# Performance work log

Measured on AMD Instinct MI355X. Metric: run time of the kernel, lower is better.

## Reference

```python
import jax, jax.numpy as jnp
import numpy as np

ATOM_DIMS = [119, 5, 12, 12, 10, 6, 6, 2, 2]  # OGB full_atom_feature_dims
N, E, D, H, L, C, G = 50000, 400000, 64, 4, 3, 10, 512
NEG_SLOPE = 0.2


def setup_inputs() -> dict:
    key = jax.random.key(0)
    ks = jax.random.split(key, 12)
    total_vocab = sum(ATOM_DIMS)  # 174
    inp = {
        "nodes_features": jax.random.randint(ks[0], (N, 9), 0, 2),
        "edges_connectivity": jax.random.randint(ks[1], (2, E), 0, N),
        "batch": jnp.sort(jax.random.randint(ks[2], (N,), 0, G)),
        "atom_emb": jax.random.normal(ks[3], (total_vocab, D), jnp.float32) * 0.1,
        # GATv2 per-layer params: lin_l (source), lin_r (target), attention vec, out bias
        "Wl": jax.random.normal(ks[4], (L, D, H * D), jnp.float32) * 0.05,
        "bl": jnp.zeros((L, H * D), jnp.float32),
        "Wr": jax.random.normal(ks[5], (L, D, H * D), jnp.float32) * 0.05,
        "br": jnp.zeros((L, H * D), jnp.float32),
        "att": jax.random.normal(ks[6], (L, H, D), jnp.float32) * 0.1,
        "gat_bias": jnp.zeros((L, D), jnp.float32),
        "Wc": jax.random.normal(ks[7], (D, C), jnp.float32) * 0.05,
        "bc": jnp.zeros((C,), jnp.float32),
    }
    return inp


def reference(nodes_features, edges_connectivity, batch, atom_emb,
              Wl, bl, Wr, br, att, gat_bias, Wc, bc):
    # --- AtomEncoder: sum of 9 categorical embeddings (tables concatenated) ---
    offsets = jnp.asarray(np.cumsum([0] + ATOM_DIMS[:-1]), dtype=nodes_features.dtype)
    x = atom_emb[nodes_features + offsets[None, :]].sum(axis=1)  # [N, D]

    # --- add self-loops (GATv2Conv default add_self_loops=True) ---
    loops = jnp.arange(N, dtype=edges_connectivity.dtype)
    src = jnp.concatenate([edges_connectivity[0], loops])  # [E+N]
    dst = jnp.concatenate([edges_connectivity[1], loops])

    for l in range(L):
        xl = (x @ Wl[l] + bl[l]).reshape(N, H, D)  # source transform
        xr = (x @ Wr[l] + br[l]).reshape(N, H, D)  # target transform
        m = jax.nn.leaky_relu(xl[src] + xr[dst], NEG_SLOPE)      # [E+N, H, D]
        e = jnp.einsum('ehd,hd->eh', m, att[l])                  # [E+N, H]
        # segment softmax over incoming edges of each target node
        emax = jax.ops.segment_max(e, dst, num_segments=N)       # [N, H]
        ea = jnp.exp(e - emax[dst])
        denom = jax.ops.segment_sum(ea, dst, num_segments=N)
        alpha = ea / denom[dst]                                  # [E+N, H]
        out = jax.ops.segment_sum(alpha[:, :, None] * xl[src], dst, num_segments=N)
        x = out.mean(axis=1) + gat_bias[l]                       # concat=False -> head mean
        if l < L - 1:
            x = jax.nn.gelu(x, approximate=False)                # nn.GELU()

    # --- global mean pool over graphs ---
    sums = jax.ops.segment_sum(x, batch, num_segments=G)         # [G, D]
    cnt = jax.ops.segment_sum(jnp.ones((N,), x.dtype), batch, num_segments=G)
    pooled = sums / jnp.maximum(cnt, 1.0)[:, None]

    return pooled @ Wc + bc                                      # [G, C]
```

## Files before the change

kernel.cpp:

```cpp
#include <hip/hip_runtime.h>
#include <hip/hip_fp16.h>
#include <math.h>

#define NEG_SLOPE 0.2f
#define LOG2E 1.44269504088896340736f

#if __has_builtin(__builtin_amdgcn_exp2f)
#define EXP2(x) __builtin_amdgcn_exp2f(x)
#else
#define EXP2(x) exp2f(x)
#endif

#define DPP_ADD(p, ctrl) \
    p += __int_as_float(__builtin_amdgcn_update_dpp(0, __float_as_int(p), ctrl, 0xf, 0xf, true))

typedef __fp16 half4v __attribute__((ext_vector_type(4)));
typedef __fp16 half2v __attribute__((ext_vector_type(2)));
typedef float  f32x4  __attribute__((ext_vector_type(4)));

__device__ __forceinline__ unsigned f2h2(float x, float y) {
    union { unsigned u; __half2 h; } r;
    r.h = __floats2half2_rn(x, y);
    return r.u;
}

#if __has_builtin(__builtin_amdgcn_fdot2)
#define FDOT2(a, b, c) __builtin_amdgcn_fdot2((a), (b), (c), false)
#else
__device__ __forceinline__ float FDOT2(half2v a, half2v b, float c) {
    return c + (float)a[0] * (float)b[0] + (float)a[1] * (float)b[1];
}
#endif

__global__ __launch_bounds__(256) void embed_kernel(
        const int* __restrict__ feat, const float* __restrict__ emb,
        const int* __restrict__ dstE, int* __restrict__ counts,
        __half* __restrict__ x, int N, int E) {
    int gid = blockIdx.x * 256 + threadIdx.x;
    if (gid < E) atomicAdd(&counts[dstE[gid]], 1);

    const int offs[9] = {0, 119, 124, 136, 148, 158, 164, 170, 172};
    int sub  = threadIdx.x >> 6;
    int lane = threadIdx.x & 63;
    int n = __builtin_amdgcn_readfirstlane(blockIdx.x * 4 + sub);
    if (n >= N) return;
    float s = 0.f;
#pragma unroll
    for (int j = 0; j < 9; ++j) {
        int idx = feat[n * 9 + j] + offs[j];
        s += emb[idx * 64 + lane];
    }
    x[(size_t)n * 64 + lane] = __float2half(s);
}

__global__ __launch_bounds__(256) void gemm_kernel(
        const __half* __restrict__ x,
        const float* __restrict__ Wl, const float* __restrict__ Wr,
        const float* __restrict__ bl, const float* __restrict__ br,
        __half* __restrict__ xl, __half* __restrict__ xr, int N) {
    int w    = threadIdx.x >> 6;
    int lane = threadIdx.x & 63;
    int lo   = lane & 15;
    int hi   = lane >> 4;
    const float* W    = blockIdx.y ? Wr : Wl;
    const float* bias = blockIdx.y ? br : bl;
    __half*      out  = blockIdx.y ? xr : xl;
    int wbase = w * 64;
    int r0    = blockIdx.x * 64;

    half4v aw[4][4];
    float4 bv[4];
#pragma unroll
    for (int mt = 0; mt < 4; ++mt) {
        int c = wbase + mt * 16 + lo;
#pragma unroll
        for (int kt = 0; kt < 4; ++kt) {
            int k = kt * 16 + hi * 4;
            float f0 = W[(size_t)(k + 0) * 256 + c];
            float f1 = W[(size_t)(k + 1) * 256 + c];
            float f2 = W[(size_t)(k + 2) * 256 + c];
            float f3 = W[(size_t)(k + 3) * 256 + c];
            half2v p0 = __builtin_amdgcn_cvt_pkrtz(f0, f1);
            half2v p1 = __builtin_amdgcn_cvt_pkrtz(f2, f3);
            aw[mt][kt][0] = p0[0]; aw[mt][kt][1] = p0[1];
            aw[mt][kt][2] = p1[0]; aw[mt][kt][3] = p1[1];
        }
        bv[mt] = *(const float4*)(bias + wbase + mt * 16 + hi * 4);
    }

    half4v xv[4][4];
#pragma unroll
    for (int nt = 0; nt < 4; ++nt) {
        int row = min(r0 + nt * 16 + lo, N - 1);
        const __half* p = x + (size_t)row * 64 + hi * 4;
#pragma unroll
        for (int kt = 0; kt < 4; ++kt)
            xv[nt][kt] = *(const half4v*)(p + kt * 16);
    }

    f32x4 acc[4][4];
#pragma unroll
    for (int mt = 0; mt < 4; ++mt)
#pragma unroll
        for (int nt = 0; nt < 4; ++nt)
            acc[mt][nt] = (f32x4){0.f, 0.f, 0.f, 0.f};

#pragma unroll
    for (int kt = 0; kt < 4; ++kt)
#pragma unroll
        for (int mt = 0; mt < 4; ++mt)
#pragma unroll
            for (int nt = 0; nt < 4; ++nt)
                acc[mt][nt] = __builtin_amdgcn_mfma_f32_16x16x16f16(
                    aw[mt][kt], xv[nt][kt], acc[mt][nt], 0, 0, 0);

#pragma unroll
    for (int nt = 0; nt < 4; ++nt) {
        int row = r0 + nt * 16 + lo;
        if (row < N) {
#pragma unroll
            for (int mt = 0; mt < 4; ++mt) {
                f32x4 a = acc[mt][nt];
                half2v p0 = __builtin_amdgcn_cvt_pkrtz(a[0] + bv[mt].x, a[1] + bv[mt].y);
                half2v p1 = __builtin_amdgcn_cvt_pkrtz(a[2] + bv[mt].z, a[3] + bv[mt].w);
                union { half2v h[2]; uint2 u; } st;
                st.h[0] = p0; st.h[1] = p1;
                int c = wbase + mt * 16 + hi * 4;
                *(uint2*)(out + (size_t)row * 256 + c) = st.u;
            }
        }
    }
}

__global__ void scan_block_kernel(const int* __restrict__ counts, int* __restrict__ excl,
                                  int* __restrict__ blockSums, int N) {
    __shared__ int lds[256];
    int b = blockIdx.x, t = threadIdx.x;
    int base = b * 1024 + t * 4;
    int v0 = (base + 0 < N) ? counts[base + 0] + 1 : 0;
    int v1 = (base + 1 < N) ? counts[base + 1] + 1 : 0;
    int v2 = (base + 2 < N) ? counts[base + 2] + 1 : 0;
    int v3 = (base + 3 < N) ? counts[base + 3] + 1 : 0;
    int s = v0 + v1 + v2 + v3;
    lds[t] = s;
    __syncthreads();
    for (int off = 1; off < 256; off <<= 1) {
        int add = (t >= off) ? lds[t - off] : 0;
        __syncthreads();
        lds[t] += add;
        __syncthreads();
    }
    int run = lds[t] - s;
    if (base + 0 < N) excl[base + 0] = run; run += v0;
    if (base + 1 < N) excl[base + 1] = run; run += v1;
    if (base + 2 < N) excl[base + 2] = run; run += v2;
    if (base + 3 < N) excl[base + 3] = run;
    if (t == 255) blockSums[b] = lds[255];
}

__global__ void scan_sums_kernel(int* __restrict__ blockSums, int nb) {
    __shared__ int lds[64];
    int t = threadIdx.x;
    int v = (t < nb) ? blockSums[t] : 0;
    lds[t] = v;
    __syncthreads();
    for (int off = 1; off < 64; off <<= 1) {
        int add = (t >= off) ? lds[t - off] : 0;
        __syncthreads();
        lds[t] += add;
        __syncthreads();
    }
    if (t < nb) blockSums[t] = lds[t] - v;
}

__global__ void finalize_kernel(int* __restrict__ csr_off, const int* __restrict__ blockSums,
                                int* __restrict__ cursor, int* __restrict__ csr_src,
                                int N, int total) {
    int i = blockIdx.x * 256 + threadIdx.x;
    if (i < N) {
        int v = csr_off[i] + blockSums[i >> 10];
        csr_off[i] = v;
        csr_src[v] = i;
        cursor[i]  = v + 1;
    }
    if (i == 0) csr_off[N] = total;
}

__global__ void scatter_kernel(const int* __restrict__ src, const int* __restrict__ dst,
                               int* __restrict__ cursor, int* __restrict__ csr_src, int E) {
    int e = blockIdx.x * 256 + threadIdx.x;
    if (e < E) {
        int pos = atomicAdd(&cursor[dst[e]], 1);
        csr_src[pos] = src[e];
    }
}

__global__ __launch_bounds__(256) void agg_kernel(
        const __half* __restrict__ xl, const __half* __restrict__ xr,
        const int* __restrict__ csr_off, const int* __restrict__ csr_src,
        const float* __restrict__ att,
        const float* __restrict__ gbias,
        __half* __restrict__ xout, int N, int apply_gelu) {
    int wave = threadIdx.x >> 6;
    int lane = threadIdx.x & 63;
    int n = __builtin_amdgcn_readfirstlane(blockIdx.x * 4 + wave);
    if (n >= N) return;

    union HU { uint2 u; half2v h[2]; };

    float4 attf = ((const float4*)att)[lane];
    half2v att_lo = __builtin_amdgcn_cvt_pkrtz(attf.x * LOG2E, attf.y * LOG2E);
    half2v att_hi = __builtin_amdgcn_cvt_pkrtz(attf.z * LOG2E, attf.w * LOG2E);

    HU xru; xru.u = *(const uint2*)(xr + (size_t)n * 256 + lane * 4);
    half2v xr_lo = xru.h[0], xr_hi = xru.h[1];
    const half2v ns2 = {(__fp16)NEG_SLOPE, (__fp16)NEG_SLOPE};

    int beg  = csr_off[n];
    int end  = csr_off[n + 1];
    int m    = end - beg;
    int last = end - 1;

    const __half* __restrict__ xlp = xl + lane * 4;

    auto idx4 = [&](int pos) -> int4 {
        int4 v;
        v.x = csr_src[min(pos,     last)];
        v.y = csr_src[min(pos + 1, last)];
        v.z = csr_src[min(pos + 2, last)];
        v.w = csr_src[min(pos + 3, last)];
        return v;
    };
    auto rows4 = [&](const int4& iv, uint2& r0, uint2& r1, uint2& r2, uint2& r3) {
        r0 = *(const uint2*)(xlp + (size_t)iv.x * 256);
        r1 = *(const uint2*)(xlp + (size_t)iv.y * 256);
        r2 = *(const uint2*)(xlp + (size_t)iv.z * 256);
        r3 = *(const uint2*)(xlp + (size_t)iv.w * 256);
    };
    auto logit = [&](half2v lo, half2v hi) -> float {
        half2v s0 = lo + xr_lo;
        half2v s1 = hi + xr_hi;
        half2v t0 = __builtin_elementwise_max(s0, s0 * ns2);
        half2v t1 = __builtin_elementwise_max(s1, s1 * ns2);
        return FDOT2(t1, att_hi, FDOT2(t0, att_lo, 0.f));
    };

    float ax = 0.f, ay = 0.f, az = 0.f, aw = 0.f, denom = 0.f;

    auto compute4 = [&](const uint2& q0, const uint2& q1, const uint2& q2,
                        const uint2& q3, int kbase) {
        HU e0, e1, e2, e3;
        e0.u = q0; e1.u = q1; e2.u = q2; e3.u = q3;
        float p0 = logit(e0.h[0], e0.h[1]);
        float p1 = logit(e1.h[0], e1.h[1]);
        float p2 = logit(e2.h[0], e2.h[1]);
        float p3 = logit(e3.h[0], e3.h[1]);
        DPP_ADD(p0, 0xB1);  DPP_ADD(p1, 0xB1);  DPP_ADD(p2, 0xB1);  DPP_ADD(p3, 0xB1);
        DPP_ADD(p0, 0x4E);  DPP_ADD(p1, 0x4E);  DPP_ADD(p2, 0x4E);  DPP_ADD(p3, 0x4E);
        DPP_ADD(p0, 0x141); DPP_ADD(p1, 0x141); DPP_ADD(p2, 0x141); DPP_ADD(p3, 0x141);
        DPP_ADD(p0, 0x140); DPP_ADD(p1, 0x140); DPP_ADD(p2, 0x140); DPP_ADD(p3, 0x140);
        float w0 = EXP2(p0);
        float w1 = (kbase + 1 < m) ? EXP2(p1) : 0.f;
        float w2 = (kbase + 2 < m) ? EXP2(p2) : 0.f;
        float w3 = (kbase + 3 < m) ? EXP2(p3) : 0.f;
        denom += (w0 + w1) + (w2 + w3);
        ax += w0 * (float)e0.h[0][0] + w1 * (float)e1.h[0][0]
            + w2 * (float)e2.h[0][0] + w3 * (float)e3.h[0][0];
        ay += w0 * (float)e0.h[0][1] + w1 * (float)e1.h[0][1]
            + w2 * (float)e2.h[0][1] + w3 * (float)e3.h[0][1];
        az += w0 * (float)e0.h[1][0] + w1 * (float)e1.h[1][0]
            + w2 * (float)e2.h[1][0] + w3 * (float)e3.h[1][0];
        aw += w0 * (float)e0.h[1][1] + w1 * (float)e1.h[1][1]
            + w2 * (float)e2.h[1][1] + w3 * (float)e3.h[1][1];
    };

    uint2 a0, a1, a2, a3, b0, b1, b2, b3, c0, c1, c2, c3;
    rows4(idx4(beg), a0, a1, a2, a3);
    if (m <= 4) {
        compute4(a0, a1, a2, a3, 0);
    } else {
        rows4(idx4(beg + 4), b0, b1, b2, b3);
        if (m <= 8) {
            compute4(a0, a1, a2, a3, 0);
            compute4(b0, b1, b2, b3, 4);
        } else {
            rows4(idx4(beg + 8), c0, c1, c2, c3);
            int4 ja = idx4(beg + 12);
            int4 jb = idx4(beg + 16);
            int4 jc = idx4(beg + 20);
            int g = 0;
            while (true) {
                compute4(a0, a1, a2, a3, g);
                if (g + 4 >= m) break;
                rows4(ja, a0, a1, a2, a3);  ja = idx4(beg + g + 24);

                compute4(b0, b1, b2, b3, g + 4);
                if (g + 8 >= m) break;
                rows4(jb, b0, b1, b2, b3);  jb = idx4(beg + g + 28);

                compute4(c0, c1, c2, c3, g + 8);
                if (g + 12 >= m) break;
                rows4(jc, c0, c1, c2, c3);  jc = idx4(beg + g + 32);

                g += 12;
            }
        }
    }

    float inv = 1.f / denom;
    float rx = ax * inv, ry = ay * inv, rz = az * inv, rw = aw * inv;
    rx += __shfl_xor(rx, 16); rx += __shfl_xor(rx, 32);
    ry += __shfl_xor(ry, 16); ry += __shfl_xor(ry, 32);
    rz += __shfl_xor(rz, 16); rz += __shfl_xor(rz, 32);
    rw += __shfl_xor(rw, 16); rw += __shfl_xor(rw, 32);

    if (lane < 16) {
        int d0 = lane * 4;
        float4 bvv = *(const float4*)(gbias + d0);
        float ox = 0.25f * rx + bvv.x;
        float oy = 0.25f * ry + bvv.y;
        float oz = 0.25f * rz + bvv.z;
        float ow = 0.25f * rw + bvv.w;
        if (apply_gelu) {
            const float kk = 0.70710678118654752440f;
            ox = 0.5f * ox * (1.f + erff(ox * kk));
            oy = 0.5f * oy * (1.f + erff(oy * kk));
            oz = 0.5f * oz * (1.f + erff(oz * kk));
            ow = 0.5f * ow * (1.f + erff(ow * kk));
        }
        uint2 st = make_uint2(f2h2(ox, oy), f2h2(oz, ow));
        *(uint2*)(xout + (size_t)n * 64 + d0) = st;
    }
}

__global__ __launch_bounds__(256) void pool_kernel(
        const __half* __restrict__ x, const int* __restrict__ batch,
        const float* __restrict__ Wc, const float* __restrict__ bc,
        float* __restrict__ out, int N, int G) {
    __shared__ float part[4][64];
    __shared__ float pooled[64];
    int g = blockIdx.x, t = threadIdx.x;
    int sub = t >> 6, lane = t & 63;
    int lo = 0, hi = N;
    while (lo < hi) { int mid = (lo + hi) >> 1; if (batch[mid] < g) lo = mid + 1; else hi = mid; }
    int beg = lo;
    hi = N;
    while (lo < hi) { int mid = (lo + hi) >> 1; if (batch[mid] < g + 1) lo = mid + 1; else hi = mid; }
    int end = lo;

    float acc = 0.f;
    for (int n = beg + sub; n < end; n += 4) acc += __half2float(x[(size_t)n * 64 + lane]);
    part[sub][lane] = acc;
    __syncthreads();
    if (t < 64) {
        float s = (part[0][t] + part[1][t]) + (part[2][t] + part[3][t]);
        int cnt = end - beg;
        pooled[t] = (cnt > 0) ? s / (float)cnt : 0.f;
    }
    __syncthreads();
    if (t < 10) {
        float o = bc[t];
        for (int d = 0; d < 64; ++d) o += pooled[d] * Wc[d * 10 + t];
        out[(size_t)g * 10 + t] = o;
    }
}

extern "C" void kernel_launch(void* const* d_in, const int* in_sizes, int n_in,
                              void* d_out, int out_size, void* d_ws, size_t ws_size,
                              hipStream_t stream) {
    const int*   feat  = (const int*)d_in[0];
    const int*   edges = (const int*)d_in[1];
    const int*   batch = (const int*)d_in[2];
    const float* emb   = (const float*)d_in[3];
    const float* Wl    = (const float*)d_in[4];
    const float* bl    = (const float*)d_in[5];
    const float* Wr    = (const float*)d_in[6];
    const float* br    = (const float*)d_in[7];
    const float* att   = (const float*)d_in[8];
    const float* gb    = (const float*)d_in[9];
    const float* Wc    = (const float*)d_in[10];
    const float* bc    = (const float*)d_in[11];
    float* out = (float*)d_out;

    const int N = in_sizes[2];
    const int E = in_sizes[1] / 2;
    const int G = out_size / 10;

    char* ws = (char*)d_ws;
    size_t off = 0;
    auto alloc = [&](size_t bytes) -> char* {
        char* p = ws + off;
        off = (off + bytes + 255) & ~(size_t)255;
        return p;
    };
    __half* x         = (__half*)alloc((size_t)N * 64 * 2);
    __half* xl        = (__half*)alloc((size_t)N * 256 * 2);
    __half* xr        = (__half*)alloc((size_t)N * 256 * 2);
    int*    counts    = (int*)alloc((size_t)N * 4);
    int*    csr_off   = (int*)alloc((size_t)(N + 8) * 4);
    int*    cursor    = (int*)alloc((size_t)N * 4);
    int*    csr_src   = (int*)alloc((size_t)(E + N + 64) * 4);
    int*    blockSums = (int*)alloc(256 * 4);

    const int* srcv = edges;
    const int* dstv = edges + E;

    hipMemsetAsync(counts, 0, (size_t)N * 4, stream);
    hipLaunchKernelGGL(embed_kernel, dim3((N + 3) / 4), dim3(256), 0, stream,
                       feat, emb, dstv, counts, x, N, E);

    int nb = (N + 1023) / 1024;
    hipLaunchKernelGGL(scan_block_kernel, dim3(nb), dim3(256), 0, stream, counts, csr_off, blockSums, N);
    hipLaunchKernelGGL(scan_sums_kernel, dim3(1), dim3(64), 0, stream, blockSums, nb);
    hipLaunchKernelGGL(finalize_kernel, dim3((N + 255) / 256), dim3(256), 0, stream,
                       csr_off, blockSums, cursor, csr_src, N, E + N);
    hipLaunchKernelGGL(scatter_kernel, dim3((E + 255) / 256), dim3(256), 0, stream, srcv, dstv, cursor, csr_src, E);

    int nchunks = (N + 63) / 64;
    for (int l = 0; l < 3; ++l) {
        hipLaunchKernelGGL(gemm_kernel, dim3(nchunks, 2), dim3(256), 0, stream,
                           x, Wl + (size_t)l * 64 * 256, Wr + (size_t)l * 64 * 256,
                           bl + l * 256, br + l * 256, xl, xr, N);
        hipLaunchKernelGGL(agg_kernel, dim3((N + 3) / 4), dim3(256), 0, stream,
                           xl, xr, csr_off, csr_src, att + l * 256, gb + l * 64,
                           x, N, (l < 2) ? 1 : 0);
    }

    hipLaunchKernelGGL(pool_kernel, dim3(G), dim3(256), 0, stream, x, batch, Wc, bc, out, N, G);
}
```

Before: 361.3 us.

## Pre-transpose weights to fp16 and compute both projections per GEMM block

Adds a small kernel that converts Wl/Wr to fp16 once per call, transposed so each lane can fetch its MFMA operand with one vector load instead of four strided scalar float loads. The GEMM grid drops its second dimension: each block loads its x tile once and loops over both the source and target projections. This halves the reads of x and cuts per-block weight-load cost. The trade-offs are one extra launch and half as many blocks, so there is less parallelism in the GEMM.

```diff
diff --git a/kernel.cpp b/kernel.cpp
--- a/kernel.cpp
+++ b/kernel.cpp
@@ -53,40 +53,30 @@
     x[(size_t)n * 64 + lane] = __float2half(s);
 }
 
+__global__ __launch_bounds__(256) void wprep_kernel(
+        const float* __restrict__ Wl, const float* __restrict__ Wr,
+        __half* __restrict__ Wt) {
+    int b = blockIdx.x;
+    int l = b >> 1, m = b & 1;
+    const float* src = (m ? Wr : Wl) + (size_t)l * 64 * 256;
+    __half* dst = Wt + (size_t)b * 256 * 64;
+    for (int i = threadIdx.x; i < 64 * 256; i += 256) {
+        int k = i >> 8;
+        int c = i & 255;
+        dst[(size_t)c * 64 + k] = __float2half(src[i]);
+    }
+}
+
 __global__ __launch_bounds__(256) void gemm_kernel(
-        const __half* __restrict__ x,
-        const float* __restrict__ Wl, const float* __restrict__ Wr,
+        const __half* __restrict__ x, const __half* __restrict__ Wt,
         const float* __restrict__ bl, const float* __restrict__ br,
         __half* __restrict__ xl, __half* __restrict__ xr, int N) {
     int w    = threadIdx.x >> 6;
     int lane = threadIdx.x & 63;
     int lo   = lane & 15;
     int hi   = lane >> 4;
-    const float* W    = blockIdx.y ? Wr : Wl;
-    const float* bias = blockIdx.y ? br : bl;
-    __half*      out  = blockIdx.y ? xr : xl;
     int wbase = w * 64;
     int r0    = blockIdx.x * 64;
-
-    half4v aw[4][4];
-    float4 bv[4];
-#pragma unroll
-    for (int mt = 0; mt < 4; ++mt) {
-        int c = wbase + mt * 16 + lo;
-#pragma unroll
-        for (int kt = 0; kt < 4; ++kt) {
-            int k = kt * 16 + hi * 4;
-            float f0 = W[(size_t)(k + 0) * 256 + c];
-            float f1 = W[(size_t)(k + 1) * 256 + c];
-            float f2 = W[(size_t)(k + 2) * 256 + c];
-            float f3 = W[(size_t)(k + 3) * 256 + c];
-            half2v p0 = __builtin_amdgcn_cvt_pkrtz(f0, f1);
-            half2v p1 = __builtin_amdgcn_cvt_pkrtz(f2, f3);
-            aw[mt][kt][0] = p0[0]; aw[mt][kt][1] = p0[1];
-            aw[mt][kt][2] = p1[0]; aw[mt][kt][3] = p1[1];
-        }
-        bv[mt] = *(const float4*)(bias + wbase + mt * 16 + hi * 4);
-    }
 
     half4v xv[4][4];
 #pragma unroll
@@ -98,35 +88,53 @@
             xv[nt][kt] = *(const half4v*)(p + kt * 16);
     }
 
-    f32x4 acc[4][4];
-#pragma unroll
-    for (int mt = 0; mt < 4; ++mt)
-#pragma unroll
-        for (int nt = 0; nt < 4; ++nt)
-            acc[mt][nt] = (f32x4){0.f, 0.f, 0.f, 0.f};
-
-#pragma unroll
-    for (int kt = 0; kt < 4; ++kt)
+#pragma unroll 1
+    for (int ct = 0; ct < 2; ++ct) {
+        const __half* Wm   = Wt + (size_t)ct * 256 * 64;
+        const float*  bias = ct ? br : bl;
+        __half*       out  = ct ? xr : xl;
+
+        half4v aw[4][4];
+        float4 bv[4];
+#pragma unroll
+        for (int mt = 0; mt < 4; ++mt) {
+            int c = wbase + mt * 16 + lo;
+#pragma unroll
+            for (int kt = 0; kt < 4; ++kt)
+                aw[mt][kt] = *(const half4v*)(Wm + (size_t)c * 64 + kt * 16 + hi * 4);
+            bv[mt] = *(const float4*)(bias + wbase + mt * 16 + hi * 4);
+        }
+
+        f32x4 acc[4][4];
 #pragma unroll
         for (int mt = 0; mt < 4; ++mt)
 #pragma unroll
             for (int nt = 0; nt < 4; ++nt)
-                acc[mt][nt] = __builtin_amdgcn_mfma_f32_16x16x16f16(
-                    aw[mt][kt], xv[nt][kt], acc[mt][nt], 0, 0, 0);
-
-#pragma unroll
-    for (int nt = 0; nt < 4; ++nt) {
-        int row = r0 + nt * 16 + lo;
-        if (row < N) {
-#pragma unroll
-            for (int mt = 0; mt < 4; ++mt) {
-                f32x4 a = acc[mt][nt];
-                half2v p0 = __builtin_amdgcn_cvt_pkrtz(a[0] + bv[mt].x, a[1] + bv[mt].y);
-                half2v p1 = __builtin_amdgcn_cvt_pkrtz(a[2] + bv[mt].z, a[3] + bv[mt].w);
-                union { half2v h[2]; uint2 u; } st;
-                st.h[0] = p0; st.h[1] = p1;
-                int c = wbase + mt * 16 + hi * 4;
-                *(uint2*)(out + (size_t)row * 256 + c) = st.u;
+                acc[mt][nt] = (f32x4){0.f, 0.f, 0.f, 0.f};
+
+#pragma unroll
+        for (int kt = 0; kt < 4; ++kt)
+#pragma unroll
+            for (int mt = 0; mt < 4; ++mt)
+#pragma unroll
+                for (int nt = 0; nt < 4; ++nt)
+                    acc[mt][nt] = __builtin_amdgcn_mfma_f32_16x16x16f16(
+                        aw[mt][kt], xv[nt][kt], acc[mt][nt], 0, 0, 0);
+
+#pragma unroll
+        for (int nt = 0; nt < 4; ++nt) {
+            int row = r0 + nt * 16 + lo;
+            if (row < N) {
+#pragma unroll
+                for (int mt = 0; mt < 4; ++mt) {
+                    f32x4 a = acc[mt][nt];
+                    half2v p0 = __builtin_amdgcn_cvt_pkrtz(a[0] + bv[mt].x, a[1] + bv[mt].y);
+                    half2v p1 = __builtin_amdgcn_cvt_pkrtz(a[2] + bv[mt].z, a[3] + bv[mt].w);
+                    union { half2v h[2]; uint2 u; } st;
+                    st.h[0] = p0; st.h[1] = p1;
+                    int c = wbase + mt * 16 + hi * 4;
+                    *(uint2*)(out + (size_t)row * 256 + c) = st.u;
+                }
             }
         }
     }
@@ -396,6 +404,7 @@
     __half* x         = (__half*)alloc((size_t)N * 64 * 2);
     __half* xl        = (__half*)alloc((size_t)N * 256 * 2);
     __half* xr        = (__half*)alloc((size_t)N * 256 * 2);
+    __half* Wt        = (__half*)alloc((size_t)6 * 256 * 64 * 2);
     int*    counts    = (int*)alloc((size_t)N * 4);
     int*    csr_off   = (int*)alloc((size_t)(N + 8) * 4);
     int*    cursor    = (int*)alloc((size_t)N * 4);
@@ -404,6 +413,8 @@
 
     const int* srcv = edges;
     const int* dstv = edges + E;
+
+    hipLaunchKernelGGL(wprep_kernel, dim3(6), dim3(256), 0, stream, Wl, Wr, Wt);
 
     hipMemsetAsync(counts, 0, (size_t)N * 4, stream);
     hipLaunchKernelGGL(embed_kernel, dim3((N + 3) / 4), dim3(256), 0, stream,
@@ -418,8 +429,8 @@
 
     int nchunks = (N + 63) / 64;
     for (int l = 0; l < 3; ++l) {
-        hipLaunchKernelGGL(gemm_kernel, dim3(nchunks, 2), dim3(256), 0, stream,
-                           x, Wl + (size_t)l * 64 * 256, Wr + (size_t)l * 64 * 256,
+        hipLaunchKernelGGL(gemm_kernel, dim3(nchunks), dim3(256), 0, stream,
+                           x, Wt + (size_t)l * 2 * 256 * 64,
                            bl + l * 256, br + l * 256, xl, xr, N);
         hipLaunchKernelGGL(agg_kernel, dim3((N + 3) / 4), dim3(256), 0, stream,
                            xl, xr, csr_off, csr_src, att + l * 256, gb + l * 64,
```

After: 384.5 us. +6.4%, slower.
